# Performance work log

Measured on AMD Instinct MI355X. Metric: run time of the kernel, lower is better.

The kernel has to match this reference:

```python
import jax, jax.numpy as jnp
import numpy as np

B, S, L, H, D, DF = 2, 1024, 2, 8, 512, 2048
DK = D // H  # head dim (dk == dv == 64)
EPS = 1e-5


def _ln(x, g, b):
    m = jnp.mean(x, axis=-1, keepdims=True)
    v = jnp.mean((x - m) ** 2, axis=-1, keepdims=True)
    return (x - m) / jnp.sqrt(v + EPS) * g + b


def setup_inputs() -> dict:
    key = jax.random.key(0)
    ks = jax.random.split(key, 8)
    sd = 1.0 / np.sqrt(D)
    sf = 1.0 / np.sqrt(DF)
    inp = {
        "src": jax.random.normal(ks[0], (B, S, D), jnp.float32),
        "Wq": jax.random.normal(ks[1], (L, D, D), jnp.float32) * sd,
        "bq": jnp.zeros((L, D), jnp.float32),
        "Wk": jax.random.normal(ks[2], (L, D, D), jnp.float32) * sd,
        "bk": jnp.zeros((L, D), jnp.float32),
        "Wv": jax.random.normal(ks[3], (L, D, D), jnp.float32) * sd,
        "bv": jnp.zeros((L, D), jnp.float32),
        "Wo": jax.random.normal(ks[4], (L, D, D), jnp.float32) * sd,
        "bo": jnp.zeros((L, D), jnp.float32),
        "W1": jax.random.normal(ks[5], (L, D, DF), jnp.float32) * sd,
        "b1": jnp.zeros((L, DF), jnp.float32),
        "W2": jax.random.normal(ks[6], (L, DF, D), jnp.float32) * sf,
        "b2": jnp.zeros((L, D), jnp.float32),
        "g1": jnp.ones((L, D), jnp.float32),
        "be1": jnp.zeros((L, D), jnp.float32),
        "g2": jnp.ones((L, D), jnp.float32),
        "be2": jnp.zeros((L, D), jnp.float32),
        "gf": jnp.ones((D,), jnp.float32),
        "bef": jnp.zeros((D,), jnp.float32),
    }
    return inp


def _heads(x):
    # [B,S,D] -> [B,H,S,DK]
    return x.reshape(B, S, H, DK).transpose(0, 2, 1, 3)


def _causal_linear_attention(q, k, v):
    # Faithful to torch: cumsum of per-step KV outer products, then query contraction.
    kv = jnp.einsum("bhsk,bhsv->bhskv", k, v)      # [B,H,S,DK,DK]
    cum = jnp.cumsum(kv, axis=2)                     # prefix sums over sequence
    return jnp.einsum("bhsk,bhskv->bhsv", q, cum)   # [B,H,S,DK]


def reference(src, Wq, bq, Wk, bk, Wv, bv, Wo, bo, W1, b1, W2, b2,
              g1, be1, g2, be2, gf, bef):
    x = src
    for i in range(L):
        q = _heads(x @ Wq[i] + bq[i])
        k = _heads(x @ Wk[i] + bk[i])
        v = _heads(x @ Wv[i] + bv[i])
        att = _causal_linear_attention(q, k, v)
        att = att.transpose(0, 2, 1, 3).reshape(B, S, D)
        att = att @ Wo[i] + bo[i]
        x = _ln(x + att, g1[i], be1[i])              # post-norm (normalize_before=False)
        ff = jax.nn.relu(x @ W1[i] + b1[i]) @ W2[i] + b2[i]
        x = _ln(x + ff, g2[i], be2[i])
    return _ln(x, gf, bef)                            # final encoder LayerNorm
```

## Files before the change

kernel.cpp:

```cpp
#include <hip/hip_runtime.h>
#include <hip/hip_bf16.h>

#define DEV static __device__ __forceinline__

typedef __attribute__((ext_vector_type(8))) short short8;
typedef __attribute__((ext_vector_type(4))) float f32x4;

DEV unsigned short f2b(float f){
  unsigned int u = __float_as_uint(f);
  return (unsigned short)((u + 0x7FFFu + ((u >> 16) & 1u)) >> 16);
}
DEV float b2f(unsigned short h){ return __uint_as_float(((unsigned int)h) << 16); }
DEV float load_in(const void* p, size_t i, int isbf){
  return isbf ? b2f(((const unsigned short*)p)[i]) : ((const float*)p)[i];
}
DEV void load_lds16(const unsigned short* g, unsigned short* l){
  __builtin_amdgcn_global_load_lds(
      (const __attribute__((address_space(1))) void*)g,
      (__attribute__((address_space(3))) void*)l, 16, 0, 0);
}

DEV int detect_isbf_block(const void* src){
  __shared__ int cnt[4];
  int tid = threadIdx.x;
  float v = b2f(((const unsigned short*)src)[2 * tid]);
  float av = fabsf(v);
  bool sane = ((av < 64.0f) && (av > 9.5e-7f)) || (v == 0.0f);
  unsigned long long m = __ballot(sane);
  if ((tid & 63) == 0) cnt[tid >> 6] = __popcll(m);
  __syncthreads();
  int tot = cnt[0] + cnt[1] + cnt[2] + cnt[3];
  __syncthreads();
  return tot > 128;
}

struct WDesc { const void* src; long src_off; unsigned short* dst; int K; int N; int tstart; };
struct WParams { WDesc d[12]; const void* dsrc; };

__global__ __launch_bounds__(256) void ingest_weights(WParams P){
  __shared__ float tile[32][33];
  int isbf = detect_isbf_block(P.dsrc);
  int b = blockIdx.x;
  int t = 0;
  #pragma unroll
  for (int i = 1; i < 12; ++i) if (b >= P.d[i].tstart) t = i;
  WDesc d = P.d[t];
  int r = b - d.tstart;
  int tiles_x = d.N >> 5;
  int tx = r % tiles_x, ty = r / tiles_x;
  int lx = threadIdx.x & 31, ly = threadIdx.x >> 5;
  #pragma unroll
  for (int i = 0; i < 4; ++i){
    int row = ty*32 + ly + i*8;
    int col = tx*32 + lx;
    tile[ly + i*8][lx] = load_in(d.src, (size_t)d.src_off + (size_t)row*d.N + col, isbf);
  }
  __syncthreads();
  #pragma unroll
  for (int i = 0; i < 4; ++i){
    int orow = tx*32 + ly + i*8;
    int ocol = ty*32 + lx;
    d.dst[(size_t)orow*d.K + ocol] = f2b(tile[lx][ly + i*8]);
  }
}

struct SDesc { const void* src; int src_off; int dstart; };
struct SParams { SDesc d[22]; float* dst; int total; };

__global__ __launch_bounds__(256) void ingest_misc(SParams S, const void* src,
                                                   float* xf, unsigned short* xb){
  int isbf = detect_isbf_block(src);
  int b = blockIdx.x, tid = threadIdx.x;
  if (b < 4096){
    int i = b*256 + tid;
    float v = load_in(src, (size_t)i, isbf);
    xf[i] = v; xb[i] = f2b(v);
  } else {
    int i = (b - 4096)*256 + tid;
    if (i < S.total){
      int t = 0;
      #pragma unroll
      for (int j = 1; j < 22; ++j) if (i >= S.d[j].dstart) t = j;
      S.dst[i] = load_in(S.d[t].src, (size_t)S.d[t].src_off + (i - S.d[t].dstart), isbf);
    }
  }
}

struct GemmArgs {
  const unsigned short* A;
  const unsigned short* Bt;
  const float* bias;
  float* Cf;
  unsigned short* Cb;
  int K;
  int lda, ldb, ldc;
  int cshift, cmask;
  size_t cstride;
  size_t cfz;
  int relu;
};

template<int BN>
__global__ __launch_bounds__(256) void gemm_bt(GemmArgs g){
  constexpr int NI = (BN == 128) ? 4 : 2;
  constexpr int NJ = 4;
  constexpr int BPASS = BN / 32;
  __shared__ __align__(16) unsigned short sA[2][128*64];
  __shared__ __align__(16) unsigned short sB[2][BN*64];
  int tid = threadIdx.x;
  int koff = blockIdx.z * g.K;
  int K = g.K, lda = g.lda, ldb = g.ldb;
  size_t bm = (size_t)blockIdx.y * 128, bn = (size_t)blockIdx.x * BN;
  int lane = tid & 63, wv = tid >> 6, quad = lane >> 4, l16 = lane & 15;
  int wm = (BN == 128) ? (wv >> 1) * 64 : wv * 32;
  int wn = (BN == 128) ? (wv & 1) * 64 : 0;
  f32x4 acc[NI][NJ];
  #pragma unroll
  for (int i=0;i<NI;++i)
    #pragma unroll
    for (int j=0;j<NJ;++j) acc[i][j] = (f32x4){0.f,0.f,0.f,0.f};
  int srow = tid >> 3;
  int schunk = (tid & 7) ^ (srow & 7);
  const unsigned short* Ap = g.A  + (bm + srow)*lda + koff + schunk*8;
  const unsigned short* Bp = g.Bt + (bn + srow)*ldb + koff + schunk*8;

  #define STAGE(buf, ko)                                                      \
    do {                                                                      \
      _Pragma("unroll")                                                       \
      for (int p = 0; p < 4; ++p)                                             \
        load_lds16(Ap + (size_t)(p*32)*lda + (ko), &sA[buf][p*2048 + tid*8]); \
      _Pragma("unroll")                                                       \
      for (int p = 0; p < BPASS; ++p)                                         \
        load_lds16(Bp + (size_t)(p*32)*ldb + (ko), &sB[buf][p*2048 + tid*8]); \
    } while (0)

  STAGE(0, 0);
  asm volatile("s_waitcnt vmcnt(0)" ::: "memory");
  __builtin_amdgcn_s_barrier();

  int nt = K >> 6;
  int cur = 0;
  for (int t = 0; t < nt; ++t){
    if (t + 1 < nt){
      STAGE(cur ^ 1, (t + 1) * 64);
      __builtin_amdgcn_sched_barrier(0);
    }
    #pragma unroll
    for (int kk = 0; kk < 2; ++kk){
      short8 af[NI], bfv[NJ];
      #pragma unroll
      for (int i=0;i<NI;++i){
        int row = wm + i*16 + l16;
        int ch  = (kk*4 + quad) ^ (row & 7);
        af[i] = *(const short8*)&sA[cur][row*64 + ch*8];
      }
      #pragma unroll
      for (int j=0;j<NJ;++j){
        int row = wn + j*16 + l16;
        int ch  = (kk*4 + quad) ^ (row & 7);
        bfv[j] = *(const short8*)&sB[cur][row*64 + ch*8];
      }
      #pragma unroll
      for (int i=0;i<NI;++i)
        #pragma unroll
        for (int j=0;j<NJ;++j)
          acc[i][j] = __builtin_amdgcn_mfma_f32_16x16x32_bf16(af[i], bfv[j], acc[i][j], 0,0,0);
    }
    if (t + 1 < nt){
      asm volatile("s_waitcnt vmcnt(0)" ::: "memory");
      __builtin_amdgcn_s_barrier();
    }
    cur ^= 1;
  }
  #undef STAGE

  float* Cf = g.Cf ? g.Cf + (size_t)blockIdx.z * g.cfz : nullptr;
  unsigned short* Cb = g.Cb;
  #pragma unroll
  for (int j=0;j<NJ;++j){
    int col = (int)bn + wn + j*16 + l16;
    float bv = g.bias ? g.bias[col] : 0.f;
    size_t cbase = ((size_t)(col >> g.cshift))*g.cstride + (col & g.cmask);
    #pragma unroll
    for (int i=0;i<NI;++i){
      #pragma unroll
      for (int r=0;r<4;++r){
        int row = (int)bm + wm + i*16 + quad*4 + r;
        float v = acc[i][j][r] + bv;
        if (g.relu) v = fmaxf(v, 0.f);
        size_t idx = cbase + (size_t)row*g.ldc;
        if (Cf) Cf[idx] = v;
        if (Cb) Cb[idx] = f2b(v);
      }
    }
  }
}

#define ATT_S 1024
#define ATT_D 512

__global__ __launch_bounds__(256) void attn_state_kernel(
    const unsigned short* k, const unsigned short* v, float* states)
{
  __shared__ __align__(16) unsigned short sVt[64*72];
  __shared__ __align__(16) unsigned short sKt[64*72];
  int tid = threadIdx.x;
  int c = blockIdx.x, bh = blockIdx.y;
  int b = bh >> 3, h = bh & 7;
  const size_t base = ((size_t)b*ATT_S + (size_t)c*64)*ATT_D + h*64;
  int lane = tid & 63, wv = tid >> 6, quad = lane >> 4, l16 = lane & 15;

  int t = lane, vc = wv*8;
  const unsigned short* vp = v + base + (size_t)t*ATT_D;
  const unsigned short* kp = k + base + (size_t)t*ATT_D;
  float4 v0 = *(const float4*)(vp + vc);
  float4 v1 = *(const float4*)(vp + vc + 32);
  float4 k0 = *(const float4*)(kp + vc);
  float4 k1 = *(const float4*)(kp + vc + 32);
  {
    const unsigned short* pv0 = (const unsigned short*)&v0;
    const unsigned short* pv1 = (const unsigned short*)&v1;
    const unsigned short* pk0 = (const unsigned short*)&k0;
    const unsigned short* pk1 = (const unsigned short*)&k1;
    #pragma unroll
    for (int e = 0; e < 8; ++e){
      sVt[(vc+e)*72 + t]    = pv0[e];
      sVt[(vc+32+e)*72 + t] = pv1[e];
      sKt[(vc+e)*72 + t]    = pk0[e];
      sKt[(vc+32+e)*72 + t] = pk1[e];
    }
  }
  __syncthreads();

  f32x4 acc[4];
  #pragma unroll
  for (int j=0;j<4;++j) acc[j] = (f32x4){0.f,0.f,0.f,0.f};
  #pragma unroll
  for (int kk=0;kk<2;++kk){
    short8 a = *(const short8*)&sVt[(wv*16 + l16)*72 + kk*32 + quad*8];
    #pragma unroll
    for (int j=0;j<4;++j){
      short8 bb = *(const short8*)&sKt[(j*16 + l16)*72 + kk*32 + quad*8];
      acc[j] = __builtin_amdgcn_mfma_f32_16x16x32_bf16(a, bb, acc[j], 0,0,0);
    }
  }
  float* st = states + ((size_t)bh*16 + c)*4096;
  #pragma unroll
  for (int j=0;j<4;++j)
    #pragma unroll
    for (int rr=0;rr<4;++rr)
      st[(wv*16 + quad*4 + rr)*64 + j*16 + l16] = acc[j][rr];
}

__global__ __launch_bounds__(256) void attn_out_kernel(
    const unsigned short* q, const unsigned short* k, const unsigned short* v,
    const float* states, unsigned short* att)
{
  __shared__ __align__(16) unsigned short sQ [64*72];
  __shared__ __align__(16) unsigned short sK [64*72];
  __shared__ __align__(16) unsigned short sVt[64*72];
  __shared__ __align__(16) float sKV[64*68];
  int tid = threadIdx.x;
  int c = blockIdx.x, bh = blockIdx.y;
  int b = bh >> 3, h = bh & 7;
  const size_t base = ((size_t)b*ATT_S + (size_t)c*64)*ATT_D + h*64;
  int lane = tid & 63, wv = tid >> 6, quad = lane >> 4, l16 = lane & 15;

  float4 racc[4];
  #pragma unroll
  for (int u=0;u<4;++u) racc[u] = (float4){0.f,0.f,0.f,0.f};
  const float* sbase = states + (size_t)bh*16*4096;
  for (int cc = 0; cc < c; ++cc){
    const float4* sp = (const float4*)(sbase + (size_t)cc*4096);
    #pragma unroll
    for (int u=0;u<4;++u){
      float4 t4 = sp[tid + u*256];
      racc[u].x += t4.x; racc[u].y += t4.y; racc[u].z += t4.z; racc[u].w += t4.w;
    }
  }
  #pragma unroll
  for (int u=0;u<4;++u){
    int e = (tid + u*256)*4;
    int row = e >> 6, col = e & 63;
    *(float4*)&sKV[row*68 + col] = racc[u];
  }

  int r = tid >> 2, c8 = (tid & 3)*8;
  const unsigned short* qp = q + base + (size_t)r*ATT_D;
  const unsigned short* kp = k + base + (size_t)r*ATT_D;
  float4 q0 = *(const float4*)(qp + c8);
  float4 q1 = *(const float4*)(qp + c8 + 32);
  float4 k0 = *(const float4*)(kp + c8);
  float4 k1 = *(const float4*)(kp + c8 + 32);
  int t = lane, vc = wv*8;
  const unsigned short* vp = v + base + (size_t)t*ATT_D;
  float4 v0 = *(const float4*)(vp + vc);
  float4 v1 = *(const float4*)(vp + vc + 32);
  *(float4*)&sQ[r*72 + c8]      = q0;
  *(float4*)&sQ[r*72 + c8 + 32] = q1;
  *(float4*)&sK[r*72 + c8]      = k0;
  *(float4*)&sK[r*72 + c8 + 32] = k1;
  {
    const unsigned short* pv0 = (const unsigned short*)&v0;
    const unsigned short* pv1 = (const unsigned short*)&v1;
    #pragma unroll
    for (int e=0;e<8;++e){
      sVt[(vc+e)*72 + t]    = pv0[e];
      sVt[(vc+32+e)*72 + t] = pv1[e];
    }
  }
  __syncthreads();

  f32x4 accS[4];
  #pragma unroll
  for (int j=0;j<4;++j) accS[j] = (f32x4){0.f,0.f,0.f,0.f};
  #pragma unroll
  for (int kk=0;kk<2;++kk){
    short8 a = *(const short8*)&sQ[(wv*16 + l16)*72 + kk*32 + quad*8];
    #pragma unroll
    for (int j=0;j<4;++j){
      short8 bb = *(const short8*)&sK[(j*16 + l16)*72 + kk*32 + quad*8];
      accS[j] = __builtin_amdgcn_mfma_f32_16x16x32_bf16(a, bb, accS[j], 0,0,0);
    }
  }
  __syncthreads();

  #pragma unroll
  for (int j=0;j<4;++j)
    #pragma unroll
    for (int rr=0;rr<4;++rr){
      int i  = wv*16 + quad*4 + rr;
      int cj = j*16 + l16;
      sK[i*72 + cj] = f2b((i >= cj) ? accS[j][rr] : 0.f);
    }

  f32x4 accO[4];
  #pragma unroll
  for (int j=0;j<4;++j) accO[j] = (f32x4){0.f,0.f,0.f,0.f};
  #pragma unroll
  for (int kk=0;kk<2;++kk){
    short8 a = *(const short8*)&sQ[(wv*16 + l16)*72 + kk*32 + quad*8];
    #pragma unroll
    for (int j=0;j<4;++j){
      const float* pf = &sKV[(j*16 + l16)*68 + kk*32 + quad*8];
      short8 bb;
      #pragma unroll
      for (int e=0;e<8;++e) ((unsigned short*)&bb)[e] = f2b(pf[e]);
      accO[j] = __builtin_amdgcn_mfma_f32_16x16x32_bf16(a, bb, accO[j], 0,0,0);
    }
  }
  __syncthreads();

  #pragma unroll
  for (int kk=0;kk<2;++kk){
    short8 a = *(const short8*)&sK[(wv*16 + l16)*72 + kk*32 + quad*8];
    #pragma unroll
    for (int j=0;j<4;++j){
      short8 bb = *(const short8*)&sVt[(j*16 + l16)*72 + kk*32 + quad*8];
      accO[j] = __builtin_amdgcn_mfma_f32_16x16x32_bf16(a, bb, accO[j], 0,0,0);
    }
  }
  #pragma unroll
  for (int j=0;j<4;++j)
    #pragma unroll
    for (int rr=0;rr<4;++rr){
      int i  = wv*16 + quad*4 + rr;
      int cj = j*16 + l16;
      att[base + (size_t)i*ATT_D + cj] = f2b(accO[j][rr]);
    }
}

__global__ __launch_bounds__(256) void add_ln_kernel(
    const float* x, const float* p, int np, const float* bias,
    const float* g, const float* bta,
    float* outf, unsigned short* outb, void* outd, const void* dsrc, int rows)
{
  int isbf = 0;
  if (dsrc) isbf = detect_isbf_block(dsrc);
  int row = blockIdx.x*4 + (threadIdx.x >> 6);
  int lane = threadIdx.x & 63;
  if (row >= rows) return;
  const float* xr = x + (size_t)row*512;
  float a[8];
  *(float4*)&a[0] = *(const float4*)(xr + lane*4);
  *(float4*)&a[4] = *(const float4*)(xr + 256 + lane*4);
  for (int s = 0; s < np; ++s){
    const float* pr = p + (size_t)s*1048576 + (size_t)row*512;
    float yb[8];
    *(float4*)&yb[0] = *(const float4*)(pr + lane*4);
    *(float4*)&yb[4] = *(const float4*)(pr + 256 + lane*4);
    #pragma unroll
    for (int e=0;e<8;++e) a[e] += yb[e];
  }
  if (bias){
    float bb2[8];
    *(float4*)&bb2[0] = *(const float4*)(bias + lane*4);
    *(float4*)&bb2[4] = *(const float4*)(bias + 256 + lane*4);
    #pragma unroll
    for (int e=0;e<8;++e) a[e] += bb2[e];
  }
  float s = 0.f, qq = 0.f;
  #pragma unroll
  for (int e=0;e<8;++e){ s += a[e]; qq += a[e]*a[e]; }
  #pragma unroll
  for (int off=32; off>0; off>>=1){
    s  += __shfl_xor(s,  off, 64);
    qq += __shfl_xor(qq, off, 64);
  }
  float mean = s * (1.f/512.f);
  float var  = qq * (1.f/512.f) - mean*mean;
  float rstd = rsqrtf(var + 1e-5f);
  float gg[8], bb[8];
  *(float4*)&gg[0] = *(const float4*)(g + lane*4);
  *(float4*)&gg[4] = *(const float4*)(g + 256 + lane*4);
  *(float4*)&bb[0] = *(const float4*)(bta + lane*4);
  *(float4*)&bb[4] = *(const float4*)(bta + 256 + lane*4);
  #pragma unroll
  for (int e=0;e<8;++e) a[e] = (a[e]-mean)*rstd*gg[e] + bb[e];
  if (outf){
    float* orow = outf + (size_t)row*512;
    *(float4*)(orow + lane*4)       = *(float4*)&a[0];
    *(float4*)(orow + 256 + lane*4) = *(float4*)&a[4];
  }
  if (outb){
    unsigned short* orow = outb + (size_t)row*512;
    #pragma unroll
    for (int e=0;e<4;++e){ orow[lane*4+e] = f2b(a[e]); orow[256+lane*4+e] = f2b(a[4+e]); }
  }
  if (outd){
    if (isbf){
      unsigned short* od = (unsigned short*)outd + (size_t)row*512;
      #pragma unroll
      for (int e=0;e<4;++e){ od[lane*4+e] = f2b(a[e]); od[256+lane*4+e] = f2b(a[4+e]); }
    } else {
      float* od = (float*)outd + (size_t)row*512;
      *(float4*)(od + lane*4)       = *(float4*)&a[0];
      *(float4*)(od + 256 + lane*4) = *(float4*)&a[4];
    }
  }
}

extern "C" void kernel_launch(void* const* d_in, const int* in_sizes, int n_in,
                              void* d_out, int out_size, void* d_ws, size_t ws_size,
                              hipStream_t stream)
{
  (void)in_sizes; (void)n_in; (void)out_size; (void)ws_size;
  const void* src = d_in[0];
  const void* Wq = d_in[1];  const void* bq = d_in[2];
  const void* Wk = d_in[3];  const void* bk = d_in[4];
  const void* Wv = d_in[5];  const void* bv = d_in[6];
  const void* Wo = d_in[7];  const void* bo = d_in[8];
  const void* W1 = d_in[9];  const void* b1 = d_in[10];
  const void* W2 = d_in[11]; const void* b2 = d_in[12];
  const void* g1 = d_in[13]; const void* be1 = d_in[14];
  const void* g2 = d_in[15]; const void* be2 = d_in[16];
  const void* gf = d_in[17]; const void* bef = d_in[18];

  char* W = (char*)d_ws;
  float* smalls          = (float*)(W + 256);
  unsigned short* wt     = (unsigned short*)(W + 65536);
  float* x_f             = (float*)(W + 12648448);
  unsigned short* x_b    = (unsigned short*)(W + 16842752);
  unsigned short* q_b    = (unsigned short*)(W + 18939904);
  unsigned short* att_b  = (unsigned short*)(W + 25231360);
  float* pp              = (float*)(W + 27328512);
  unsigned short* h1_b   = (unsigned short*)(W + 44105728);
  float* states          = (float*)(W + 44105728);
  unsigned short* k_b = q_b + 1048576;
  unsigned short* v_b = q_b + 2097152;

  WParams wp;
  {
    const void* wsrc[6] = {Wq, Wk, Wv, Wo, W1, W2};
    int wK[6] = {512,512,512,512,512,2048};
    int wN[6] = {512,512,512,512,2048,512};
    long wsz[6] = {262144,262144,262144,262144,1048576,1048576};
    int tstart = 0; size_t dsto = 0;
    for (int l=0;l<2;++l)
      for (int ti=0;ti<6;++ti){
        int idx = l*6+ti;
        wp.d[idx].src = wsrc[ti];
        wp.d[idx].src_off = (long)l * wsz[ti];
        wp.d[idx].dst = wt + dsto;
        wp.d[idx].K = wK[ti]; wp.d[idx].N = wN[ti];
        wp.d[idx].tstart = tstart;
        tstart += (wK[ti]/32)*(wN[ti]/32);
        dsto += (size_t)wsz[ti];
      }
    wp.dsrc = src;
    ingest_weights<<<dim3(6144), 256, 0, stream>>>(wp);
  }

  SParams sp;
  {
    const void* ss[10] = {bq,bk,bv,bo,b1,b2,g1,be1,g2,be2};
    int slen[10] = {512,512,512,512,2048,512,512,512,512,512};
    int dcur = 0, di = 0;
    for (int l=0;l<2;++l)
      for (int ti=0;ti<10;++ti){
        sp.d[di].src = ss[ti];
        sp.d[di].src_off = l * slen[ti];
        sp.d[di].dstart = dcur;
        dcur += slen[ti]; ++di;
      }
    sp.d[20].src = gf;  sp.d[20].src_off = 0; sp.d[20].dstart = dcur; dcur += 512;
    sp.d[21].src = bef; sp.d[21].src_off = 0; sp.d[21].dstart = dcur; dcur += 512;
    sp.dst = smalls; sp.total = dcur;
    ingest_misc<<<dim3(4152), 256, 0, stream>>>(sp, src, x_f, x_b);
  }

  for (int l = 0; l < 2; ++l){
    unsigned short* WqkvT = wt + (size_t)l*3145728;
    unsigned short* WoT   = WqkvT + 786432;
    unsigned short* W1T   = WqkvT + 1048576;
    unsigned short* W2T   = WqkvT + 2097152;
    float* base  = smalls + l*6656;
    float* p_bqkv= base;
    float* p_bo  = base + 1536;
    float* p_b1  = base + 2048;
    float* p_b2  = base + 4096;
    float* p_g1  = base + 4608;
    float* p_be1 = base + 5120;
    float* p_g2  = base + 5632;
    float* p_be2 = base + 6144;

    GemmArgs qkv = {};
    qkv.A = x_b; qkv.Bt = WqkvT; qkv.bias = p_bqkv;
    qkv.Cf = nullptr; qkv.Cb = q_b;
    qkv.K = 512; qkv.lda = 512; qkv.ldb = 512; qkv.ldc = 512;
    qkv.cshift = 9; qkv.cmask = 511; qkv.cstride = 1048576; qkv.cfz = 0; qkv.relu = 0;
    gemm_bt<64><<<dim3(24,16,1), 256, 0, stream>>>(qkv);

    attn_state_kernel<<<dim3(16,16), 256, 0, stream>>>(k_b, v_b, states);
    attn_out_kernel<<<dim3(16,16), 256, 0, stream>>>(q_b, k_b, v_b, states, att_b);

    GemmArgs go = {};
    go.A = att_b; go.Bt = WoT; go.bias = nullptr;
    go.Cf = pp; go.Cb = nullptr;
    go.K = 256; go.lda = 512; go.ldb = 512; go.ldc = 512;
    go.cshift = 30; go.cmask = 0x3fffffff; go.cstride = 0; go.cfz = 1048576; go.relu = 0;
    gemm_bt<64><<<dim3(8,16,2), 256, 0, stream>>>(go);

    add_ln_kernel<<<dim3(512), 256, 0, stream>>>(x_f, pp, 2, p_bo, p_g1, p_be1,
                                                 x_f, x_b, nullptr, nullptr, 2048);

    GemmArgs f1 = {};
    f1.A = x_b; f1.Bt = W1T; f1.bias = p_b1;
    f1.Cf = nullptr; f1.Cb = h1_b;
    f1.K = 512; f1.lda = 512; f1.ldb = 512; f1.ldc = 2048;
    f1.cshift = 30; f1.cmask = 0x3fffffff; f1.cstride = 0; f1.cfz = 0; f1.relu = 1;
    gemm_bt<128><<<dim3(16,16,1), 256, 0, stream>>>(f1);

    GemmArgs f2 = {};
    f2.A = h1_b; f2.Bt = W2T; f2.bias = nullptr;
    f2.Cf = pp; f2.Cb = nullptr;
    f2.K = 512; f2.lda = 2048; f2.ldb = 2048; f2.ldc = 512;
    f2.cshift = 30; f2.cmask = 0x3fffffff; f2.cstride = 0; f2.cfz = 1048576; f2.relu = 0;
    gemm_bt<64><<<dim3(8,16,4), 256, 0, stream>>>(f2);

    add_ln_kernel<<<dim3(512), 256, 0, stream>>>(x_f, pp, 4, p_b2, p_g2, p_be2,
                                                 x_f, x_b, nullptr, nullptr, 2048);
  }

  add_ln_kernel<<<dim3(512), 256, 0, stream>>>(x_f, nullptr, 0, nullptr,
                                               smalls + 13312, smalls + 13824,
                                               nullptr, nullptr, d_out, src, 2048);
}
```

Measured before the change: 264.8 us.

## Fuse attention state and output kernels with flag-based inter-block sync, merge ingest kernels

Merges the two weight/misc ingest kernels into one launch, which also zeroes a flag array. Fuses the per-chunk KV state computation into the attention output kernel: each block writes its chunk state, publishes a release flag, then spin-waits on flags for earlier chunks before summing their prefix states. Also halves the split-K factor of the second FFN GEMM (K per split 512 to 1024, 4 splits to 2), which cuts partial-sum traffic in the following add+LN. The cost is that inter-block spinning relies on all 256 blocks being co-resident to avoid deadlock, and the smaller FFN2 grid gives less parallelism.

```diff
diff --git a/kernel.cpp b/kernel.cpp
--- a/kernel.cpp
+++ b/kernel.cpp
@@ -35,53 +35,60 @@
 }
 
 struct WDesc { const void* src; long src_off; unsigned short* dst; int K; int N; int tstart; };
-struct WParams { WDesc d[12]; const void* dsrc; };
-
-__global__ __launch_bounds__(256) void ingest_weights(WParams P){
+struct SDesc { const void* src; int src_off; int dstart; };
+struct IngestParams {
+  WDesc w[12];
+  SDesc s[22];
+  float* sdst; int stotal;
+  const void* src;
+  float* xf; unsigned short* xb;
+  int* flags;
+};
+
+__global__ __launch_bounds__(256) void ingest_all(IngestParams P){
   __shared__ float tile[32][33];
-  int isbf = detect_isbf_block(P.dsrc);
-  int b = blockIdx.x;
-  int t = 0;
-  #pragma unroll
-  for (int i = 1; i < 12; ++i) if (b >= P.d[i].tstart) t = i;
-  WDesc d = P.d[t];
-  int r = b - d.tstart;
-  int tiles_x = d.N >> 5;
-  int tx = r % tiles_x, ty = r / tiles_x;
-  int lx = threadIdx.x & 31, ly = threadIdx.x >> 5;
-  #pragma unroll
-  for (int i = 0; i < 4; ++i){
-    int row = ty*32 + ly + i*8;
-    int col = tx*32 + lx;
-    tile[ly + i*8][lx] = load_in(d.src, (size_t)d.src_off + (size_t)row*d.N + col, isbf);
-  }
-  __syncthreads();
-  #pragma unroll
-  for (int i = 0; i < 4; ++i){
-    int orow = tx*32 + ly + i*8;
-    int ocol = ty*32 + lx;
-    d.dst[(size_t)orow*d.K + ocol] = f2b(tile[lx][ly + i*8]);
-  }
-}
-
-struct SDesc { const void* src; int src_off; int dstart; };
-struct SParams { SDesc d[22]; float* dst; int total; };
-
-__global__ __launch_bounds__(256) void ingest_misc(SParams S, const void* src,
-                                                   float* xf, unsigned short* xb){
-  int isbf = detect_isbf_block(src);
   int b = blockIdx.x, tid = threadIdx.x;
-  if (b < 4096){
-    int i = b*256 + tid;
-    float v = load_in(src, (size_t)i, isbf);
-    xf[i] = v; xb[i] = f2b(v);
+  if (b >= 10296){
+    P.flags[tid] = 0; P.flags[tid + 256] = 0;
+    return;
+  }
+  int isbf = detect_isbf_block(P.src);
+  if (b < 6144){
+    int t = 0;
+    #pragma unroll
+    for (int i = 1; i < 12; ++i) if (b >= P.w[i].tstart) t = i;
+    WDesc d = P.w[t];
+    int r = b - d.tstart;
+    int tiles_x = d.N >> 5;
+    int tx = r % tiles_x, ty = r / tiles_x;
+    int lx = tid & 31, ly = tid >> 5;
+    #pragma unroll
+    for (int i = 0; i < 4; ++i){
+      int row = ty*32 + ly + i*8;
+      int col = tx*32 + lx;
+      tile[ly + i*8][lx] = load_in(d.src, (size_t)d.src_off + (size_t)row*d.N + col, isbf);
+    }
+    __syncthreads();
+    #pragma unroll
+    for (int i = 0; i < 4; ++i){
+      int orow = tx*32 + ly + i*8;
+      int ocol = ty*32 + lx;
+      d.dst[(size_t)orow*d.K + ocol] = f2b(tile[lx][ly + i*8]);
+    }
+    return;
+  }
+  int mb = b - 6144;
+  if (mb < 4096){
+    int i = mb*256 + tid;
+    float v = load_in(P.src, (size_t)i, isbf);
+    P.xf[i] = v; P.xb[i] = f2b(v);
   } else {
-    int i = (b - 4096)*256 + tid;
-    if (i < S.total){
+    int i = (mb - 4096)*256 + tid;
+    if (i < P.stotal){
       int t = 0;
       #pragma unroll
-      for (int j = 1; j < 22; ++j) if (i >= S.d[j].dstart) t = j;
-      S.dst[i] = load_in(S.d[t].src, (size_t)S.d[t].src_off + (i - S.d[t].dstart), isbf);
+      for (int j = 1; j < 22; ++j) if (i >= P.s[j].dstart) t = j;
+      P.sdst[i] = load_in(P.s[t].src, (size_t)P.s[t].src_off + (i - P.s[t].dstart), isbf);
     }
   }
 }
@@ -199,65 +206,13 @@
 #define ATT_S 1024
 #define ATT_D 512
 
-__global__ __launch_bounds__(256) void attn_state_kernel(
-    const unsigned short* k, const unsigned short* v, float* states)
-{
-  __shared__ __align__(16) unsigned short sVt[64*72];
-  __shared__ __align__(16) unsigned short sKt[64*72];
-  int tid = threadIdx.x;
-  int c = blockIdx.x, bh = blockIdx.y;
-  int b = bh >> 3, h = bh & 7;
-  const size_t base = ((size_t)b*ATT_S + (size_t)c*64)*ATT_D + h*64;
-  int lane = tid & 63, wv = tid >> 6, quad = lane >> 4, l16 = lane & 15;
-
-  int t = lane, vc = wv*8;
-  const unsigned short* vp = v + base + (size_t)t*ATT_D;
-  const unsigned short* kp = k + base + (size_t)t*ATT_D;
-  float4 v0 = *(const float4*)(vp + vc);
-  float4 v1 = *(const float4*)(vp + vc + 32);
-  float4 k0 = *(const float4*)(kp + vc);
-  float4 k1 = *(const float4*)(kp + vc + 32);
-  {
-    const unsigned short* pv0 = (const unsigned short*)&v0;
-    const unsigned short* pv1 = (const unsigned short*)&v1;
-    const unsigned short* pk0 = (const unsigned short*)&k0;
-    const unsigned short* pk1 = (const unsigned short*)&k1;
-    #pragma unroll
-    for (int e = 0; e < 8; ++e){
-      sVt[(vc+e)*72 + t]    = pv0[e];
-      sVt[(vc+32+e)*72 + t] = pv1[e];
-      sKt[(vc+e)*72 + t]    = pk0[e];
-      sKt[(vc+32+e)*72 + t] = pk1[e];
-    }
-  }
-  __syncthreads();
-
-  f32x4 acc[4];
-  #pragma unroll
-  for (int j=0;j<4;++j) acc[j] = (f32x4){0.f,0.f,0.f,0.f};
-  #pragma unroll
-  for (int kk=0;kk<2;++kk){
-    short8 a = *(const short8*)&sVt[(wv*16 + l16)*72 + kk*32 + quad*8];
-    #pragma unroll
-    for (int j=0;j<4;++j){
-      short8 bb = *(const short8*)&sKt[(j*16 + l16)*72 + kk*32 + quad*8];
-      acc[j] = __builtin_amdgcn_mfma_f32_16x16x32_bf16(a, bb, acc[j], 0,0,0);
-    }
-  }
-  float* st = states + ((size_t)bh*16 + c)*4096;
-  #pragma unroll
-  for (int j=0;j<4;++j)
-    #pragma unroll
-    for (int rr=0;rr<4;++rr)
-      st[(wv*16 + quad*4 + rr)*64 + j*16 + l16] = acc[j][rr];
-}
-
-__global__ __launch_bounds__(256) void attn_out_kernel(
+__global__ __launch_bounds__(256) void attn_fused_kernel(
     const unsigned short* q, const unsigned short* k, const unsigned short* v,
-    const float* states, unsigned short* att)
+    float* states, int* flags, unsigned short* att)
 {
   __shared__ __align__(16) unsigned short sQ [64*72];
   __shared__ __align__(16) unsigned short sK [64*72];
+  __shared__ __align__(16) unsigned short sKt[64*72];
   __shared__ __align__(16) unsigned short sVt[64*72];
   __shared__ __align__(16) float sKV[64*68];
   int tid = threadIdx.x;
@@ -265,25 +220,6 @@
   int b = bh >> 3, h = bh & 7;
   const size_t base = ((size_t)b*ATT_S + (size_t)c*64)*ATT_D + h*64;
   int lane = tid & 63, wv = tid >> 6, quad = lane >> 4, l16 = lane & 15;
-
-  float4 racc[4];
-  #pragma unroll
-  for (int u=0;u<4;++u) racc[u] = (float4){0.f,0.f,0.f,0.f};
-  const float* sbase = states + (size_t)bh*16*4096;
-  for (int cc = 0; cc < c; ++cc){
-    const float4* sp = (const float4*)(sbase + (size_t)cc*4096);
-    #pragma unroll
-    for (int u=0;u<4;++u){
-      float4 t4 = sp[tid + u*256];
-      racc[u].x += t4.x; racc[u].y += t4.y; racc[u].z += t4.z; racc[u].w += t4.w;
-    }
-  }
-  #pragma unroll
-  for (int u=0;u<4;++u){
-    int e = (tid + u*256)*4;
-    int row = e >> 6, col = e & 63;
-    *(float4*)&sKV[row*68 + col] = racc[u];
-  }
 
   int r = tid >> 2, c8 = (tid & 3)*8;
   const unsigned short* qp = q + base + (size_t)r*ATT_D;
@@ -294,8 +230,11 @@
   float4 k1 = *(const float4*)(kp + c8 + 32);
   int t = lane, vc = wv*8;
   const unsigned short* vp = v + base + (size_t)t*ATT_D;
+  const unsigned short* kp2 = k + base + (size_t)t*ATT_D;
   float4 v0 = *(const float4*)(vp + vc);
   float4 v1 = *(const float4*)(vp + vc + 32);
+  float4 kc0 = *(const float4*)(kp2 + vc);
+  float4 kc1 = *(const float4*)(kp2 + vc + 32);
   *(float4*)&sQ[r*72 + c8]      = q0;
   *(float4*)&sQ[r*72 + c8 + 32] = q1;
   *(float4*)&sK[r*72 + c8]      = k0;
@@ -303,13 +242,43 @@
   {
     const unsigned short* pv0 = (const unsigned short*)&v0;
     const unsigned short* pv1 = (const unsigned short*)&v1;
+    const unsigned short* pk0 = (const unsigned short*)&kc0;
+    const unsigned short* pk1 = (const unsigned short*)&kc1;
     #pragma unroll
     for (int e=0;e<8;++e){
       sVt[(vc+e)*72 + t]    = pv0[e];
       sVt[(vc+32+e)*72 + t] = pv1[e];
-    }
-  }
-  __syncthreads();
+      sKt[(vc+e)*72 + t]    = pk0[e];
+      sKt[(vc+32+e)*72 + t] = pk1[e];
+    }
+  }
+  __syncthreads();
+
+  {
+    f32x4 accst[4];
+    #pragma unroll
+    for (int j=0;j<4;++j) accst[j] = (f32x4){0.f,0.f,0.f,0.f};
+    #pragma unroll
+    for (int kk=0;kk<2;++kk){
+      short8 a = *(const short8*)&sVt[(wv*16 + l16)*72 + kk*32 + quad*8];
+      #pragma unroll
+      for (int j=0;j<4;++j){
+        short8 bb = *(const short8*)&sKt[(j*16 + l16)*72 + kk*32 + quad*8];
+        accst[j] = __builtin_amdgcn_mfma_f32_16x16x32_bf16(a, bb, accst[j], 0,0,0);
+      }
+    }
+    float* st = states + ((size_t)bh*16 + c)*4096;
+    #pragma unroll
+    for (int j=0;j<4;++j)
+      #pragma unroll
+      for (int rr=0;rr<4;++rr)
+        st[(wv*16 + quad*4 + rr)*64 + j*16 + l16] = accst[j][rr];
+  }
+  __syncthreads();
+  if (tid == 0){
+    __threadfence();
+    __hip_atomic_store(&flags[bh*16 + c], 1, __ATOMIC_RELEASE, __HIP_MEMORY_SCOPE_AGENT);
+  }
 
   f32x4 accS[4];
   #pragma unroll
@@ -334,6 +303,33 @@
       sK[i*72 + cj] = f2b((i >= cj) ? accS[j][rr] : 0.f);
     }
 
+  if (tid == 0){
+    for (int cc = 0; cc < c; ++cc)
+      while (__hip_atomic_load(&flags[bh*16 + cc], __ATOMIC_ACQUIRE,
+                               __HIP_MEMORY_SCOPE_AGENT) == 0){}
+  }
+  __syncthreads();
+
+  float4 racc[4];
+  #pragma unroll
+  for (int u=0;u<4;++u) racc[u] = (float4){0.f,0.f,0.f,0.f};
+  const float* sbase = states + (size_t)bh*16*4096;
+  for (int cc = 0; cc < c; ++cc){
+    const float4* sp = (const float4*)(sbase + (size_t)cc*4096);
+    #pragma unroll
+    for (int u=0;u<4;++u){
+      float4 t4 = sp[tid + u*256];
+      racc[u].x += t4.x; racc[u].y += t4.y; racc[u].z += t4.z; racc[u].w += t4.w;
+    }
+  }
+  #pragma unroll
+  for (int u=0;u<4;++u){
+    int e = (tid + u*256)*4;
+    int row = e >> 6, col = e & 63;
+    *(float4*)&sKV[row*68 + col] = racc[u];
+  }
+  __syncthreads();
+
   f32x4 accO[4];
   #pragma unroll
   for (int j=0;j<4;++j) accO[j] = (f32x4){0.f,0.f,0.f,0.f};
@@ -349,8 +345,6 @@
       accO[j] = __builtin_amdgcn_mfma_f32_16x16x32_bf16(a, bb, accO[j], 0,0,0);
     }
   }
-  __syncthreads();
-
   #pragma unroll
   for (int kk=0;kk<2;++kk){
     short8 a = *(const short8*)&sK[(wv*16 + l16)*72 + kk*32 + quad*8];
@@ -466,10 +460,11 @@
   float* pp              = (float*)(W + 27328512);
   unsigned short* h1_b   = (unsigned short*)(W + 44105728);
   float* states          = (float*)(W + 44105728);
+  int* flags             = (int*)(W + 52494336);
   unsigned short* k_b = q_b + 1048576;
   unsigned short* v_b = q_b + 2097152;
 
-  WParams wp;
+  IngestParams ip;
   {
     const void* wsrc[6] = {Wq, Wk, Wv, Wo, W1, W2};
     int wK[6] = {512,512,512,512,512,2048};
@@ -479,34 +474,29 @@
     for (int l=0;l<2;++l)
       for (int ti=0;ti<6;++ti){
         int idx = l*6+ti;
-        wp.d[idx].src = wsrc[ti];
-        wp.d[idx].src_off = (long)l * wsz[ti];
-        wp.d[idx].dst = wt + dsto;
-        wp.d[idx].K = wK[ti]; wp.d[idx].N = wN[ti];
-        wp.d[idx].tstart = tstart;
+        ip.w[idx].src = wsrc[ti];
+        ip.w[idx].src_off = (long)l * wsz[ti];
+        ip.w[idx].dst = wt + dsto;
+        ip.w[idx].K = wK[ti]; ip.w[idx].N = wN[ti];
+        ip.w[idx].tstart = tstart;
         tstart += (wK[ti]/32)*(wN[ti]/32);
         dsto += (size_t)wsz[ti];
       }
-    wp.dsrc = src;
-    ingest_weights<<<dim3(6144), 256, 0, stream>>>(wp);
-  }
-
-  SParams sp;
-  {
     const void* ss[10] = {bq,bk,bv,bo,b1,b2,g1,be1,g2,be2};
     int slen[10] = {512,512,512,512,2048,512,512,512,512,512};
     int dcur = 0, di = 0;
     for (int l=0;l<2;++l)
       for (int ti=0;ti<10;++ti){
-        sp.d[di].src = ss[ti];
-        sp.d[di].src_off = l * slen[ti];
-        sp.d[di].dstart = dcur;
+        ip.s[di].src = ss[ti];
+        ip.s[di].src_off = l * slen[ti];
+        ip.s[di].dstart = dcur;
         dcur += slen[ti]; ++di;
       }
-    sp.d[20].src = gf;  sp.d[20].src_off = 0; sp.d[20].dstart = dcur; dcur += 512;
-    sp.d[21].src = bef; sp.d[21].src_off = 0; sp.d[21].dstart = dcur; dcur += 512;
-    sp.dst = smalls; sp.total = dcur;
-    ingest_misc<<<dim3(4152), 256, 0, stream>>>(sp, src, x_f, x_b);
+    ip.s[20].src = gf;  ip.s[20].src_off = 0; ip.s[20].dstart = dcur; dcur += 512;
+    ip.s[21].src = bef; ip.s[21].src_off = 0; ip.s[21].dstart = dcur; dcur += 512;
+    ip.sdst = smalls; ip.stotal = dcur;
+    ip.src = src; ip.xf = x_f; ip.xb = x_b; ip.flags = flags;
+    ingest_all<<<dim3(10297), 256, 0, stream>>>(ip);
   }
 
   for (int l = 0; l < 2; ++l){
@@ -531,8 +521,8 @@
     qkv.cshift = 9; qkv.cmask = 511; qkv.cstride = 1048576; qkv.cfz = 0; qkv.relu = 0;
     gemm_bt<64><<<dim3(24,16,1), 256, 0, stream>>>(qkv);
 
-    attn_state_kernel<<<dim3(16,16), 256, 0, stream>>>(k_b, v_b, states);
-    attn_out_kernel<<<dim3(16,16), 256, 0, stream>>>(q_b, k_b, v_b, states, att_b);
+    attn_fused_kernel<<<dim3(16,16), 256, 0, stream>>>(q_b, k_b, v_b, states,
+                                                       flags + l*256, att_b);
 
     GemmArgs go = {};
     go.A = att_b; go.Bt = WoT; go.bias = nullptr;
@@ -554,11 +544,11 @@
     GemmArgs f2 = {};
     f2.A = h1_b; f2.Bt = W2T; f2.bias = nullptr;
     f2.Cf = pp; f2.Cb = nullptr;
-    f2.K = 512; f2.lda = 2048; f2.ldb = 2048; f2.ldc = 512;
+    f2.K = 1024; f2.lda = 2048; f2.ldb = 2048; f2.ldc = 512;
     f2.cshift = 30; f2.cmask = 0x3fffffff; f2.cstride = 0; f2.cfz = 1048576; f2.relu = 0;
-    gemm_bt<64><<<dim3(8,16,4), 256, 0, stream>>>(f2);
-
-    add_ln_kernel<<<dim3(512), 256, 0, stream>>>(x_f, pp, 4, p_b2, p_g2, p_be2,
+    gemm_bt<64><<<dim3(8,16,2), 256, 0, stream>>>(f2);
+
+    add_ln_kernel<<<dim3(512), 256, 0, stream>>>(x_f, pp, 2, p_b2, p_g2, p_be2,
                                                  x_f, x_b, nullptr, nullptr, 2048);
   }
 
```

New measurement: 327.0 us. 23.5% more time.
